# Kernel optimization log

Measured on AMD Instinct MI355X. Metric: run time of the kernel, lower is better.

The kernel has to match this reference:

```python
import jax, jax.numpy as jnp
import numpy as np

B, S, D, K, F = 4, 2048, 1024, 4, 4096
C_COEF = 8.0  # RG-LRU gating exponent from Griffin paper
EPS = 1e-6


def setup_inputs() -> dict:
    key = jax.random.key(0)
    ks = jax.random.split(key, 12)
    def n(k, shape, scale=1.0):
        return jax.random.normal(k, shape, dtype=jnp.float32) * scale
    sd = 1.0 / np.sqrt(D)
    return {
        "x": n(ks[0], (B, S, D)),
        "velocity": n(ks[1], (B, S, D), 0.1),
        "pre_norm_w": jnp.ones((D,), jnp.float32),
        "conv_kernel": n(ks[2], (D, K), 0.3),   # depthwise causal conv weights
        "conv_bias": jnp.zeros((D,), jnp.float32),
        "W_gate": n(ks[3], (D, D), sd),
        "W_a": n(ks[4], (D, D), sd),
        "lam": n(ks[5], (D,)),
        "W_out": n(ks[6], (2 * D, D), 1.0 / np.sqrt(2 * D)),
        "b_out": jnp.zeros((D,), jnp.float32),
        "log_beta": n(ks[7], (D,), 0.5),
        "ffn_norm_w": jnp.ones((D,), jnp.float32),
        "W_ff1": n(ks[8], (D, F), sd),
        "b_ff1": jnp.zeros((F,), jnp.float32),
        "W_ff2": n(ks[9], (F, D), 1.0 / np.sqrt(F)),
        "b_ff2": jnp.zeros((D,), jnp.float32),
    }


def _rmsnorm(x, w):
    # matches: rsqrt(x.float().pow(2).mean(-1, keepdim=True) + 1e-6); cast back; * weight
    xf = x.astype(jnp.float32)
    rms = jax.lax.rsqrt(jnp.mean(xf * xf, axis=-1, keepdims=True) + EPS)
    return (xf * rms).astype(x.dtype) * w


def _causal_dwconv(x, kernel, bias):
    # y[b,t,d] = bias[d] + sum_k kernel[d,k] * x[b,t-k,d]  (causal depthwise)
    k_taps = kernel.shape[1]
    s = x.shape[1]
    pad = jnp.pad(x, ((0, 0), (k_taps - 1, 0), (0, 0)))
    out = bias
    for k in range(k_taps):  # tiny fixed loop over kernel taps
        out = out + pad[:, k_taps - 1 - k : k_taps - 1 - k + s, :] * kernel[:, k]
    return out


def _griffin_scan(x, W_gate, W_a, lam):
    # RG-LRU: h_t = a_t * h_{t-1} + sqrt(1 - a_t^2) * (i_t * x_t)
    gate = jax.nn.sigmoid(jnp.einsum("bsd,de->bse", x, W_gate))
    log_a = -C_COEF * jax.nn.softplus(lam) * jax.nn.sigmoid(
        jnp.einsum("bsd,de->bse", x, W_a)
    )  # [B,S,D], log_a <= 0
    a = jnp.exp(log_a)
    u = jnp.sqrt(jnp.maximum(1.0 - a * a, 0.0)) * (gate * x)

    def step(h, au):
        a_t, u_t = au
        h = a_t * h + u_t
        return h, h

    a_t = jnp.moveaxis(a, 1, 0)  # [S,B,D]
    u_t = jnp.moveaxis(u, 1, 0)
    h0 = jnp.zeros_like(a_t[0])
    _, hs = jax.lax.scan(step, h0, (a_t, u_t))
    return jnp.moveaxis(hs, 0, 1)  # [B,S,D]


def reference(x, velocity, pre_norm_w, conv_kernel, conv_bias, W_gate, W_a, lam,
              W_out, b_out, log_beta, ffn_norm_w, W_ff1, b_ff1, W_ff2, b_ff2):
    x_norm = _rmsnorm(x, pre_norm_w)
    conv_out = _causal_dwconv(x_norm, conv_kernel, conv_bias)
    griffin_out = _griffin_scan(x_norm, W_gate, W_a, lam)
    mixer_out = jnp.concatenate([conv_out, griffin_out], axis=-1) @ W_out + b_out
    beta = jax.nn.sigmoid(log_beta)
    velocity = beta * velocity + mixer_out
    x = x + velocity
    normed = _rmsnorm(x, ffn_norm_w)
    ffn = jax.nn.gelu(normed @ W_ff1 + b_ff1) @ W_ff2 + b_ff2
    return (x + ffn, velocity)
```

## Files before the change

kernel.cpp:

```cpp
#include <hip/hip_runtime.h>

static constexpr int Bb = 4;
static constexpr int Ss = 2048;
static constexpr int Dd = 1024;
static constexpr int Ff = 4096;
static constexpr int Mm = Bb * Ss;
static constexpr size_t ND = (size_t)Mm * Dd;
static constexpr int CH = 32;
static constexpr int CL = Ss / CH;

typedef __attribute__((ext_vector_type(8))) short short8;
typedef __attribute__((ext_vector_type(4))) float floatx4;

__device__ __forceinline__ unsigned f2bf(float f) {
  unsigned u = __builtin_bit_cast(unsigned, f);
  return (u + 0x7FFFu + ((u >> 16) & 1u)) >> 16;
}
__device__ __forceinline__ float bf2f(unsigned bits) {
  return __builtin_bit_cast(float, bits << 16);
}
__device__ __forceinline__ void gload_lds16(const void* g, void* lds) {
  __builtin_amdgcn_global_load_lds((const __attribute__((address_space(1))) void*)g,
                                   (__attribute__((address_space(3))) void*)lds,
                                   16, 0, 0);
}
__device__ __forceinline__ float fsig(float x) {
  return __builtin_amdgcn_rcpf(1.0f + __expf(-x));
}
__device__ __forceinline__ float fgelu(float v) {
  float z = 1.5957691216057308f * fmaf(0.044715f * v, v * v, v);
  return v * __builtin_amdgcn_rcpf(1.0f + __expf(-z));
}

__global__ __launch_bounds__(256) void wconv_k(const float* __restrict__ W,
                                               unsigned short* __restrict__ WT,
                                               int K, int N) {
  __shared__ float tile[32][33];
  int tx = threadIdx.x & 31, ty = threadIdx.x >> 5;
  int bx = blockIdx.x * 32, by = blockIdx.y * 32;
#pragma unroll
  for (int i = 0; i < 32; i += 8)
    tile[ty + i][tx] = W[(size_t)(by + ty + i) * N + bx + tx];
  __syncthreads();
#pragma unroll
  for (int i = 0; i < 32; i += 8)
    WT[(size_t)(bx + ty + i) * K + by + tx] = (unsigned short)f2bf(tile[tx][ty + i]);
}

__global__ __launch_bounds__(256) void rmsnorm_bf_k(const float* __restrict__ x,
                                                    const float* __restrict__ w,
                                                    unsigned short* __restrict__ out) {
  int row = blockIdx.x;
  const float4* xr = (const float4*)(x + (size_t)row * Dd);
  int t = threadIdx.x;
  float4 v = xr[t];
  float ss = v.x * v.x + v.y * v.y + v.z * v.z + v.w * v.w;
#pragma unroll
  for (int off = 32; off > 0; off >>= 1) ss += __shfl_down(ss, off, 64);
  __shared__ float sb[4];
  if ((t & 63) == 0) sb[t >> 6] = ss;
  __syncthreads();
  float tot = sb[0] + sb[1] + sb[2] + sb[3];
  float sc = rsqrtf(tot * (1.0f / (float)Dd) + 1e-6f);
  float4 wv = ((const float4*)w)[t];
  unsigned lo = f2bf(v.x * sc * wv.x) | (f2bf(v.y * sc * wv.y) << 16);
  unsigned hi = f2bf(v.z * sc * wv.z) | (f2bf(v.w * sc * wv.w) << 16);
  *(uint2*)(out + (size_t)row * Dd + t * 4) = make_uint2(lo, hi);
}

__global__ __launch_bounds__(256) void conv_k(const unsigned short* __restrict__ xn,
                                              const float* __restrict__ kern,
                                              const float* __restrict__ bias,
                                              unsigned short* __restrict__ outC) {
  size_t q = (size_t)blockIdx.x * 256 + threadIdx.x;
  size_t i = q * 4;
  int d = (int)(i & (Dd - 1));
  int m = (int)(i >> 10);
  int t = m & (Ss - 1);
  float acc[4];
#pragma unroll
  for (int j = 0; j < 4; j++) acc[j] = bias[d + j];
#pragma unroll
  for (int k = 0; k < 4; k++) {
    if (t >= k) {
      uint2 xv = *(const uint2*)(xn + i - (size_t)k * Dd);
      float x0 = bf2f(xv.x & 0xFFFF), x1 = bf2f(xv.x >> 16);
      float x2 = bf2f(xv.y & 0xFFFF), x3 = bf2f(xv.y >> 16);
      acc[0] = fmaf(kern[(d + 0) * 4 + k], x0, acc[0]);
      acc[1] = fmaf(kern[(d + 1) * 4 + k], x1, acc[1]);
      acc[2] = fmaf(kern[(d + 2) * 4 + k], x2, acc[2]);
      acc[3] = fmaf(kern[(d + 3) * 4 + k], x3, acc[3]);
    }
  }
  unsigned lo = f2bf(acc[0]) | (f2bf(acc[1]) << 16);
  unsigned hi = f2bf(acc[2]) | (f2bf(acc[3]) << 16);
  *(uint2*)(outC + (size_t)m * (2 * Dd) + d) = make_uint2(lo, hi);
}

template <int MODE>
__global__ __launch_bounds__(512, 2) void bgemm3_k(const unsigned short* __restrict__ A,
                                                   const unsigned short* __restrict__ BT,
                                                   void* __restrict__ Cout,
                                                   int M, int N, int K,
                                                   const float* __restrict__ bias,
                                                   const float* __restrict__ extra,
                                                   const float* __restrict__ vel_in,
                                                   const float* __restrict__ x_in,
                                                   const float* __restrict__ log_beta,
                                                   float* __restrict__ vel_out) {
  __shared__ unsigned short LA[2][256 * 64];
  __shared__ unsigned short LB[2][256 * 64];
  const int tid = threadIdx.x;
  const int wid = tid >> 6, lane = tid & 63;
  const int wm = wid >> 2, wn = wid & 3;
  const int r = lane & 15, quad = lane >> 4, r7 = lane & 7;

  const int gx = gridDim.x;
  int id = blockIdx.y * gx + blockIdx.x;
  const int nwg = gx * gridDim.y;
  id = (id & 7) * (nwg >> 3) + (id >> 3);
  const int bm = (id / gx) * 256, bn = (id % gx) * 256;
  const int NIT = K >> 7;

  const int lrow = lane >> 3;
  const int sblk = (lane & 7) ^ lrow;
  const unsigned short* AsrcB = A  + (size_t)(bm + lrow) * K + sblk * 8;
  const unsigned short* BsrcB = BT + (size_t)(bn + lrow) * K + sblk * 8;

  const int aB = wm * 8192 + r * 64;
  const int bB = wn * 4096 + r * 64;
  const int kq0 = (quad ^ r7) * 8;
  const int kq1 = ((4 + quad) ^ r7) * 8;

  floatx4 acc[8][4];
#pragma unroll
  for (int i = 0; i < 8; i++)
#pragma unroll
    for (int j = 0; j < 4; j++) acc[i][j] = (floatx4){0.f, 0.f, 0.f, 0.f};

#define STG_A(bq, k0, h, s)                                                           \
  gload_lds16(AsrcB + (size_t)((h) * 128 + (s) * 64 + wid * 8) * K + (k0),            \
              (void*)&LA[bq][((h) * 128 + (s) * 64 + wid * 8) * 64])
#define STG_B(bq, k0, h, s)                                                           \
  gload_lds16(BsrcB + (size_t)((h) * 128 + (s) * 64 + wid * 8) * K + (k0),            \
              (void*)&LB[bq][((h) * 128 + (s) * 64 + wid * 8) * 64])
#define RDA(il, IH, buf)                                                              \
  aF[il][0] = *(const short8*)&LA[buf][aB + (IH) * 4096 + (il) * 1024 + kq0];         \
  aF[il][1] = *(const short8*)&LA[buf][aB + (IH) * 4096 + (il) * 1024 + kq1]
#define RDB(BF, jl, jg, buf)                                                          \
  BF[jl][0] = *(const short8*)&LB[buf][bB + (jg) * 1024 + kq0];                       \
  BF[jl][1] = *(const short8*)&LB[buf][bB + (jg) * 1024 + kq1]
#define MM2(il, jl, BF, IH, JH)                                                       \
  acc[(IH) * 4 + (il)][(JH) * 2 + (jl)] = __builtin_amdgcn_mfma_f32_16x16x32_bf16(    \
      BF[jl][0], aF[il][0], acc[(IH) * 4 + (il)][(JH) * 2 + (jl)], 0, 0, 0);          \
  acc[(IH) * 4 + (il)][(JH) * 2 + (jl)] = __builtin_amdgcn_mfma_f32_16x16x32_bf16(    \
      BF[jl][1], aF[il][1], acc[(IH) * 4 + (il)][(JH) * 2 + (jl)], 0, 0, 0)
#define MQUAD(BF, IH, JH)                                                             \
  MM2(0, 0, BF, IH, JH); MM2(0, 1, BF, IH, JH); MM2(1, 0, BF, IH, JH);                \
  MM2(1, 1, BF, IH, JH); MM2(2, 0, BF, IH, JH); MM2(2, 1, BF, IH, JH);                \
  MM2(3, 0, BF, IH, JH); MM2(3, 1, BF, IH, JH)
#define BAR() __builtin_amdgcn_s_barrier()
#define LGK0()                                                                        \
  asm volatile("s_waitcnt lgkmcnt(0)" ::: "memory");                                  \
  __builtin_amdgcn_sched_barrier(0)
#define PRIO(x) __builtin_amdgcn_s_setprio(x)

  STG_A(0, 0, 0, 0); STG_A(0, 0, 0, 1); STG_A(0, 0, 1, 0); STG_A(0, 0, 1, 1);
  STG_B(0, 0, 0, 0); STG_B(0, 0, 0, 1); STG_B(0, 0, 1, 0); STG_B(0, 0, 1, 1);
  STG_B(1, 64, 0, 0); STG_B(1, 64, 0, 1); STG_B(1, 64, 1, 0); STG_B(1, 64, 1, 1);
  asm volatile("s_waitcnt vmcnt(4)" ::: "memory");
  BAR();
  __builtin_amdgcn_sched_barrier(0);

  for (int it = 0; it < NIT; ++it) {
    const int T = 2 * it;
    const int pf = (it + 1 < NIT);
    const int kA1 = (T + 1) << 6;
    const int k2 = (T + 2) << 6, k3 = (T + 3) << 6;
    short8 aF[4][2], b0[2][2], b1[2][2];

    STG_A(1, kA1, 0, 0); STG_A(1, kA1, 0, 1);
    RDA(0, 0, 0); RDA(1, 0, 0); RDA(2, 0, 0); RDA(3, 0, 0);
    RDB(b0, 0, 0, 0); RDB(b0, 1, 1, 0);
    BAR(); LGK0();
    PRIO(1); MQUAD(b0, 0, 0); PRIO(0);
    BAR();

    STG_A(1, kA1, 1, 0); STG_A(1, kA1, 1, 1);
    RDB(b1, 0, 2, 0); RDB(b1, 1, 3, 0);
    BAR(); LGK0();
    PRIO(1); MQUAD(b1, 0, 1); PRIO(0);
    BAR();

    if (pf) { STG_B(0, k2, 0, 0); STG_B(0, k2, 0, 1); }
    RDA(0, 1, 0); RDA(1, 1, 0); RDA(2, 1, 0); RDA(3, 1, 0);
    BAR(); LGK0();
    PRIO(1); MQUAD(b0, 1, 0); PRIO(0);
    BAR();

    if (pf) { STG_B(0, k2, 1, 0); STG_B(0, k2, 1, 1); }
    BAR();
    PRIO(1); MQUAD(b1, 1, 1); PRIO(0);
    if (pf) asm volatile("s_waitcnt vmcnt(4)" ::: "memory");
    else    asm volatile("s_waitcnt vmcnt(0)" ::: "memory");
    BAR();
    __builtin_amdgcn_sched_barrier(0);

    if (pf) { STG_A(0, k2, 0, 0); STG_A(0, k2, 0, 1); }
    RDA(0, 0, 1); RDA(1, 0, 1); RDA(2, 0, 1); RDA(3, 0, 1);
    RDB(b0, 0, 0, 1); RDB(b0, 1, 1, 1);
    BAR(); LGK0();
    PRIO(1); MQUAD(b0, 0, 0); PRIO(0);
    BAR();

    if (pf) { STG_A(0, k2, 1, 0); STG_A(0, k2, 1, 1); }
    RDB(b1, 0, 2, 1); RDB(b1, 1, 3, 1);
    BAR(); LGK0();
    PRIO(1); MQUAD(b1, 0, 1); PRIO(0);
    BAR();

    if (pf) { STG_B(1, k3, 0, 0); STG_B(1, k3, 0, 1); }
    RDA(0, 1, 1); RDA(1, 1, 1); RDA(2, 1, 1); RDA(3, 1, 1);
    BAR(); LGK0();
    PRIO(1); MQUAD(b0, 1, 0); PRIO(0);
    BAR();

    if (pf) { STG_B(1, k3, 1, 0); STG_B(1, k3, 1, 1); }
    BAR();
    PRIO(1); MQUAD(b1, 1, 1); PRIO(0);
    if (pf) {
      asm volatile("s_waitcnt vmcnt(4)" ::: "memory");
      BAR();
      __builtin_amdgcn_sched_barrier(0);
    }
  }
#undef STG_A
#undef STG_B
#undef RDA
#undef RDB
#undef MM2
#undef MQUAD

#pragma unroll
  for (int i = 0; i < 8; i++) {
    int rowg = bm + wm * 128 + i * 16 + r;
#pragma unroll
    for (int j = 0; j < 4; j++) {
      int colg = bn + wn * 64 + j * 16 + quad * 4;
      size_t idx = (size_t)rowg * N + colg;
      float v0 = acc[i][j][0], v1 = acc[i][j][1], v2 = acc[i][j][2], v3 = acc[i][j][3];
      if (MODE & 1) {
        float4 bv = *(const float4*)(bias + colg);
        v0 += bv.x; v1 += bv.y; v2 += bv.z; v3 += bv.w;
      }
      if (MODE & 2) {
        v0 = fgelu(v0); v1 = fgelu(v1); v2 = fgelu(v2); v3 = fgelu(v3);
      }
      if (MODE & 4) {
        float4 ev = *(const float4*)(extra + idx);
        v0 += ev.x; v1 += ev.y; v2 += ev.z; v3 += ev.w;
      }
      if (MODE & 16) {
        float4 lb = *(const float4*)(log_beta + colg);
        float4 vi = *(const float4*)(vel_in + idx);
        float4 xi = *(const float4*)(x_in + idx);
        float4 vn;
        vn.x = fmaf(fsig(lb.x), vi.x, v0);
        vn.y = fmaf(fsig(lb.y), vi.y, v1);
        vn.z = fmaf(fsig(lb.z), vi.z, v2);
        vn.w = fmaf(fsig(lb.w), vi.w, v3);
        *(float4*)(vel_out + idx) = vn;
        v0 = xi.x + vn.x; v1 = xi.y + vn.y; v2 = xi.z + vn.z; v3 = xi.w + vn.w;
      }
      if (MODE & 8) {
        uint2 pk;
        pk.x = f2bf(v0) | (f2bf(v1) << 16);
        pk.y = f2bf(v2) | (f2bf(v3) << 16);
        *(uint2*)((unsigned short*)Cout + idx) = pk;
      } else {
        float4 o; o.x = v0; o.y = v1; o.z = v2; o.w = v3;
        *(float4*)((float*)Cout + idx) = o;
      }
    }
  }
}

template <int MODE>
__global__ __launch_bounds__(512, 2) void bgemm4_k(const unsigned short* __restrict__ A,
                                                   const unsigned short* __restrict__ BT,
                                                   void* __restrict__ Cout,
                                                   int M, int N, int K,
                                                   const float* __restrict__ bias,
                                                   const float* __restrict__ extra,
                                                   const float* __restrict__ vel_in,
                                                   const float* __restrict__ x_in,
                                                   const float* __restrict__ log_beta,
                                                   float* __restrict__ vel_out) {
  __shared__ unsigned short LA[2][256 * 64];
  __shared__ unsigned short LB[2][128 * 64];
  const int tid = threadIdx.x;
  const int wid = tid >> 6, lane = tid & 63;
  const int wm = wid >> 1, wn = wid & 1;
  const int r = lane & 15, quad = lane >> 4, r7 = lane & 7;

  const int gx = gridDim.x;
  int id = blockIdx.y * gx + blockIdx.x;
  const int nwg = gx * gridDim.y;
  id = (id & 7) * (nwg >> 3) + (id >> 3);
  const int bm = (id / gx) * 256, bn = (id % gx) * 128;
  const int NIT = K >> 7;

  const int lrow = lane >> 3;
  const int sblk = (lane & 7) ^ lrow;
  const unsigned short* AsrcB = A  + (size_t)(bm + lrow) * K + sblk * 8;
  const unsigned short* BsrcB = BT + (size_t)(bn + lrow) * K + sblk * 8;

  const int aB = wm * 4096 + r * 64;
  const int bB = wn * 4096 + r * 64;
  const int kq0 = (quad ^ r7) * 8;
  const int kq1 = ((4 + quad) ^ r7) * 8;

  floatx4 acc[4][4];
#pragma unroll
  for (int i = 0; i < 4; i++)
#pragma unroll
    for (int j = 0; j < 4; j++) acc[i][j] = (floatx4){0.f, 0.f, 0.f, 0.f};

#define STG_A4(bq, k0, h, s)                                                          \
  gload_lds16(AsrcB + (size_t)((h) * 128 + (s) * 64 + wid * 8) * K + (k0),            \
              (void*)&LA[bq][((h) * 128 + (s) * 64 + wid * 8) * 64])
#define STG_B4(bq, k0, s)                                                             \
  gload_lds16(BsrcB + (size_t)((s) * 64 + wid * 8) * K + (k0),                        \
              (void*)&LB[bq][((s) * 64 + wid * 8) * 64])
#define RDA4(IH, buf)                                                                 \
  aF[0][0] = *(const short8*)&LA[buf][aB + (IH) * 2048 + kq0];                        \
  aF[0][1] = *(const short8*)&LA[buf][aB + (IH) * 2048 + kq1];                        \
  aF[1][0] = *(const short8*)&LA[buf][aB + (IH) * 2048 + 1024 + kq0];                 \
  aF[1][1] = *(const short8*)&LA[buf][aB + (IH) * 2048 + 1024 + kq1]
#define RDB4(BF, JH, buf)                                                             \
  BF[0][0] = *(const short8*)&LB[buf][bB + (JH) * 2048 + kq0];                        \
  BF[0][1] = *(const short8*)&LB[buf][bB + (JH) * 2048 + kq1];                        \
  BF[1][0] = *(const short8*)&LB[buf][bB + (JH) * 2048 + 1024 + kq0];                 \
  BF[1][1] = *(const short8*)&LB[buf][bB + (JH) * 2048 + 1024 + kq1]
#define MM24(il, jl, BF, IH, JH)                                                      \
  acc[(IH) * 2 + (il)][(JH) * 2 + (jl)] = __builtin_amdgcn_mfma_f32_16x16x32_bf16(    \
      BF[jl][0], aF[il][0], acc[(IH) * 2 + (il)][(JH) * 2 + (jl)], 0, 0, 0);          \
  acc[(IH) * 2 + (il)][(JH) * 2 + (jl)] = __builtin_amdgcn_mfma_f32_16x16x32_bf16(    \
      BF[jl][1], aF[il][1], acc[(IH) * 2 + (il)][(JH) * 2 + (jl)], 0, 0, 0)
#define MQ4(BF, IH, JH)                                                               \
  MM24(0, 0, BF, IH, JH); MM24(0, 1, BF, IH, JH);                                     \
  MM24(1, 0, BF, IH, JH); MM24(1, 1, BF, IH, JH)

  STG_A4(0, 0, 0, 0); STG_A4(0, 0, 0, 1); STG_A4(0, 0, 1, 0); STG_A4(0, 0, 1, 1);
  STG_B4(0, 0, 0); STG_B4(0, 0, 1);
  STG_B4(1, 64, 0); STG_B4(1, 64, 1);
  asm volatile("s_waitcnt vmcnt(2)" ::: "memory");
  BAR();
  __builtin_amdgcn_sched_barrier(0);

  for (int it = 0; it < NIT; ++it) {
    const int T = 2 * it;
    const int pf = (it + 1 < NIT);
    const int kA1 = (T + 1) << 6;
    const int k2 = (T + 2) << 6, k3 = (T + 3) << 6;
    short8 aF[2][2], b0[2][2], b1[2][2];

    STG_A4(1, kA1, 0, 0); STG_A4(1, kA1, 0, 1);
    RDA4(0, 0); RDB4(b0, 0, 0);
    BAR(); LGK0();
    PRIO(1); MQ4(b0, 0, 0); PRIO(0);
    BAR();

    STG_A4(1, kA1, 1, 0); STG_A4(1, kA1, 1, 1);
    RDB4(b1, 1, 0);
    BAR(); LGK0();
    PRIO(1); MQ4(b1, 0, 1); PRIO(0);
    BAR();

    if (pf) STG_B4(0, k2, 0);
    RDA4(1, 0);
    BAR(); LGK0();
    PRIO(1); MQ4(b0, 1, 0); PRIO(0);
    BAR();

    if (pf) STG_B4(0, k2, 1);
    BAR();
    PRIO(1); MQ4(b1, 1, 1); PRIO(0);
    if (pf) asm volatile("s_waitcnt vmcnt(2)" ::: "memory");
    else    asm volatile("s_waitcnt vmcnt(0)" ::: "memory");
    BAR();
    __builtin_amdgcn_sched_barrier(0);

    if (pf) { STG_A4(0, k2, 0, 0); STG_A4(0, k2, 0, 1); }
    RDA4(0, 1); RDB4(b0, 0, 1);
    BAR(); LGK0();
    PRIO(1); MQ4(b0, 0, 0); PRIO(0);
    BAR();

    if (pf) { STG_A4(0, k2, 1, 0); STG_A4(0, k2, 1, 1); }
    RDB4(b1, 1, 1);
    BAR(); LGK0();
    PRIO(1); MQ4(b1, 0, 1); PRIO(0);
    BAR();

    if (pf) STG_B4(1, k3, 0);
    RDA4(1, 1);
    BAR(); LGK0();
    PRIO(1); MQ4(b0, 1, 0); PRIO(0);
    BAR();

    if (pf) STG_B4(1, k3, 1);
    BAR();
    PRIO(1); MQ4(b1, 1, 1); PRIO(0);
    if (pf) {
      asm volatile("s_waitcnt vmcnt(2)" ::: "memory");
      BAR();
      __builtin_amdgcn_sched_barrier(0);
    }
  }
#undef STG_A4
#undef STG_B4
#undef RDA4
#undef RDB4
#undef MM24
#undef MQ4
#undef BAR
#undef LGK0
#undef PRIO

#pragma unroll
  for (int i = 0; i < 4; i++) {
    int rowg = bm + wm * 64 + i * 16 + r;
#pragma unroll
    for (int j = 0; j < 4; j++) {
      int colg = bn + wn * 64 + j * 16 + quad * 4;
      size_t idx = (size_t)rowg * N + colg;
      float v0 = acc[i][j][0], v1 = acc[i][j][1], v2 = acc[i][j][2], v3 = acc[i][j][3];
      if (MODE & 1) {
        float4 bv = *(const float4*)(bias + colg);
        v0 += bv.x; v1 += bv.y; v2 += bv.z; v3 += bv.w;
      }
      if (MODE & 2) {
        v0 = fgelu(v0); v1 = fgelu(v1); v2 = fgelu(v2); v3 = fgelu(v3);
      }
      if (MODE & 4) {
        float4 ev = *(const float4*)(extra + idx);
        v0 += ev.x; v1 += ev.y; v2 += ev.z; v3 += ev.w;
      }
      if (MODE & 16) {
        float4 lb = *(const float4*)(log_beta + colg);
        float4 vi = *(const float4*)(vel_in + idx);
        float4 xi = *(const float4*)(x_in + idx);
        float4 vn;
        vn.x = fmaf(fsig(lb.x), vi.x, v0);
        vn.y = fmaf(fsig(lb.y), vi.y, v1);
        vn.z = fmaf(fsig(lb.z), vi.z, v2);
        vn.w = fmaf(fsig(lb.w), vi.w, v3);
        *(float4*)(vel_out + idx) = vn;
        v0 = xi.x + vn.x; v1 = xi.y + vn.y; v2 = xi.z + vn.z; v3 = xi.w + vn.w;
      }
      if (MODE & 8) {
        uint2 pk;
        pk.x = f2bf(v0) | (f2bf(v1) << 16);
        pk.y = f2bf(v2) | (f2bf(v3) << 16);
        *(uint2*)((unsigned short*)Cout + idx) = pk;
      } else {
        float4 o; o.x = v0; o.y = v1; o.z = v2; o.w = v3;
        *(float4*)((float*)Cout + idx) = o;
      }
    }
  }
}

__global__ __launch_bounds__(256) void scan_p1(const unsigned short* __restrict__ gapre,
                                               const unsigned short* __restrict__ xn,
                                               const float* __restrict__ lam,
                                               unsigned short* __restrict__ ub,
                                               float* __restrict__ carryA,
                                               float* __restrict__ carryH) {
  int g = blockIdx.x * 256 + threadIdx.x;
  int e = g & (Dd - 1);
  int bc = g >> 10;
  int b = bc & 3;
  int c = bc >> 2;
  float l = lam[e];
  float sp = fmaxf(l, 0.0f) + log1pf(__expf(-fabsf(l)));
  float m8sp = -8.0f * sp;
  size_t m0 = (size_t)b * Ss + (size_t)c * CL;
  float A = 1.0f, h = 0.0f;
#pragma unroll 4
  for (int t = 0; t < CL; t++) {
    size_t m = m0 + t;
    float gp = bf2f(gapre[m * 2048 + e]);
    float ap = bf2f(gapre[m * 2048 + 1024 + e]);
    float xv = bf2f(xn[m * Dd + e]);
    float a = __expf(m8sp * fsig(ap));
    float u = sqrtf(fmaxf(1.0f - a * a, 0.0f)) * fsig(gp) * xv;
    ub[m * Dd + e] = (unsigned short)f2bf(u);
    A *= a;
    h = fmaf(a, h, u);
  }
  carryA[c * 4096 + b * 1024 + e] = A;
  carryH[c * 4096 + b * 1024 + e] = h;
}

__global__ __launch_bounds__(256) void scan_p2(const float* __restrict__ carryA,
                                               const float* __restrict__ carryH,
                                               float* __restrict__ init) {
  int ch = blockIdx.x * 256 + threadIdx.x;
  float H = 0.0f;
#pragma unroll
  for (int c = 0; c < CH; c++) {
    init[c * 4096 + ch] = H;
    H = fmaf(carryA[c * 4096 + ch], H, carryH[c * 4096 + ch]);
  }
}

__global__ __launch_bounds__(256) void scan_p3(const unsigned short* __restrict__ gapre,
                                               const unsigned short* __restrict__ ub,
                                               const float* __restrict__ lam,
                                               const float* __restrict__ init,
                                               unsigned short* __restrict__ outC) {
  int g = blockIdx.x * 256 + threadIdx.x;
  int e = g & (Dd - 1);
  int bc = g >> 10;
  int b = bc & 3;
  int c = bc >> 2;
  float l = lam[e];
  float sp = fmaxf(l, 0.0f) + log1pf(__expf(-fabsf(l)));
  float m8sp = -8.0f * sp;
  size_t m0 = (size_t)b * Ss + (size_t)c * CL;
  float h = init[c * 4096 + b * 1024 + e];
#pragma unroll 4
  for (int t = 0; t < CL; t++) {
    size_t m = m0 + t;
    float ap = bf2f(gapre[m * 2048 + 1024 + e]);
    float a = __expf(m8sp * fsig(ap));
    float u = bf2f(ub[m * Dd + e]);
    h = fmaf(a, h, u);
    outC[m * (2 * Dd) + Dd + e] = (unsigned short)f2bf(h);
  }
}

extern "C" void kernel_launch(void* const* d_in, const int* in_sizes, int n_in,
                              void* d_out, int out_size, void* d_ws, size_t ws_size,
                              hipStream_t stream) {
  const float* x        = (const float*)d_in[0];
  const float* velocity = (const float*)d_in[1];
  const float* pre_w    = (const float*)d_in[2];
  const float* conv_w   = (const float*)d_in[3];
  const float* conv_b   = (const float*)d_in[4];
  const float* W_gate   = (const float*)d_in[5];
  const float* W_a      = (const float*)d_in[6];
  const float* lam      = (const float*)d_in[7];
  const float* W_out    = (const float*)d_in[8];
  const float* b_out    = (const float*)d_in[9];
  const float* log_beta = (const float*)d_in[10];
  const float* ffn_w    = (const float*)d_in[11];
  const float* W_ff1    = (const float*)d_in[12];
  const float* b_ff1    = (const float*)d_in[13];
  const float* W_ff2    = (const float*)d_in[14];
  const float* b_ff2    = (const float*)d_in[15];

  float* out0 = (float*)d_out;
  float* out1 = out0 + ND;

  const size_t MB = 1024 * 1024;
  char* ws = (char*)d_ws;
  unsigned short* WgaT  = (unsigned short*)ws;
  unsigned short* WoT   = WgaT + (size_t)2 * 1024 * 1024;
  unsigned short* Wf1T  = WoT + (size_t)2 * 1024 * 1024;
  unsigned short* Wf2T  = Wf1T + (size_t)4 * 1024 * 1024;
  float*          mixer = (float*)(ws + 24 * MB);
  float*          carA  = (float*)(ws + 24 * MB);
  float*          carH  = (float*)(ws + 24 * MB + 512 * 1024);
  float*          initb = (float*)(ws + 25 * MB);
  unsigned short* conc  = (unsigned short*)(ws + 56 * MB);
  unsigned short* gapre = (unsigned short*)(ws + 88 * MB);
  unsigned short* xnbf  = (unsigned short*)(ws + 120 * MB);
  unsigned short* ubf   = (unsigned short*)(ws + 136 * MB);
  unsigned short* midbf = (unsigned short*)(ws + 88 * MB);
  unsigned short* nrmbf = (unsigned short*)(ws + 56 * MB);

  const int EB = 256;
  const int egrid4 = (int)(ND / 4 / EB);

  wconv_k<<<dim3(32, 32),  256, 0, stream>>>(W_gate, WgaT, 1024, 1024);
  wconv_k<<<dim3(32, 32),  256, 0, stream>>>(W_a,    WgaT + (size_t)1024 * 1024, 1024, 1024);
  wconv_k<<<dim3(32, 64),  256, 0, stream>>>(W_out,  WoT, 2048, 1024);
  wconv_k<<<dim3(128, 32), 256, 0, stream>>>(W_ff1,  Wf1T, 1024, 4096);
  wconv_k<<<dim3(32, 128), 256, 0, stream>>>(W_ff2,  Wf2T, 4096, 1024);
  rmsnorm_bf_k<<<Mm, 256, 0, stream>>>(x, pre_w, xnbf);
  conv_k<<<egrid4, EB, 0, stream>>>(xnbf, conv_w, conv_b, conc);
  bgemm3_k<8><<<dim3(8, 32), 512, 0, stream>>>(xnbf, WgaT, gapre, Mm, 2048, 1024,
      nullptr, nullptr, nullptr, nullptr, nullptr, nullptr);
  scan_p1<<<512, 256, 0, stream>>>(gapre, xnbf, lam, ubf, carA, carH);
  scan_p2<<<16, 256, 0, stream>>>(carA, carH, initb);
  scan_p3<<<512, 256, 0, stream>>>(gapre, ubf, lam, initb, conc);
  bgemm4_k<1 | 16><<<dim3(8, 32), 512, 0, stream>>>(conc, WoT, mixer, Mm, 1024, 2048,
      b_out, nullptr, velocity, x, log_beta, out1);
  rmsnorm_bf_k<<<Mm, 256, 0, stream>>>(mixer, ffn_w, nrmbf);
  bgemm3_k<1 | 2 | 8><<<dim3(16, 32), 512, 0, stream>>>(nrmbf, Wf1T, midbf, Mm, 4096, 1024,
      b_ff1, nullptr, nullptr, nullptr, nullptr, nullptr);
  bgemm4_k<1 | 4><<<dim3(8, 32), 512, 0, stream>>>(midbf, Wf2T, out0, Mm, 1024, 4096,
      b_ff2, mixer, nullptr, nullptr, nullptr, nullptr);
}
```

Baseline: 587.3 us.

## Triple-buffer A tile in bgemm4 kernel with rotating LDS slots

Makes the A operand LDS staging in the 256x128 GEMM kernel a three-slot ring instead of two, so A tiles are prefetched two K-steps ahead. Each half-iteration now issues two MQ4 blocks per barrier phase instead of one, halving the number of barrier/lgkm wait points per K-step. This is meant to hide global-to-LDS latency and cut synchronisation overhead. In exchange LDS use grows by 32 KB per block (to 128 KB), which may limit occupancy at launch_bounds(512,2), and more B fragments are held in registers at once.

```diff
diff --git a/kernel.cpp b/kernel.cpp
--- a/kernel.cpp
+++ b/kernel.cpp
@@ -296,7 +296,7 @@
                                                    const float* __restrict__ x_in,
                                                    const float* __restrict__ log_beta,
                                                    float* __restrict__ vel_out) {
-  __shared__ unsigned short LA[2][256 * 64];
+  __shared__ unsigned short LA[3][256 * 64];
   __shared__ unsigned short LB[2][128 * 64];
   const int tid = threadIdx.x;
   const int wid = tid >> 6, lane = tid & 63;
@@ -315,6 +315,10 @@
   const unsigned short* AsrcB = A  + (size_t)(bm + lrow) * K + sblk * 8;
   const unsigned short* BsrcB = BT + (size_t)(bn + lrow) * K + sblk * 8;
 
+  unsigned short* ALDS = &LA[0][0];
+  unsigned short* B0 = &LB[0][0];
+  unsigned short* B1 = &LB[1][0];
+
   const int aB = wm * 4096 + r * 64;
   const int bB = wn * 4096 + r * 64;
   const int kq0 = (quad ^ r7) * 8;
@@ -326,104 +330,91 @@
 #pragma unroll
     for (int j = 0; j < 4; j++) acc[i][j] = (floatx4){0.f, 0.f, 0.f, 0.f};
 
-#define STG_A4(bq, k0, h, s)                                                          \
+#define STG_A6(dst, k0, h, s)                                                         \
   gload_lds16(AsrcB + (size_t)((h) * 128 + (s) * 64 + wid * 8) * K + (k0),            \
-              (void*)&LA[bq][((h) * 128 + (s) * 64 + wid * 8) * 64])
-#define STG_B4(bq, k0, s)                                                             \
+              (void*)((dst) + ((h) * 128 + (s) * 64 + wid * 8) * 64))
+#define STG_B6(dst, k0, s)                                                            \
   gload_lds16(BsrcB + (size_t)((s) * 64 + wid * 8) * K + (k0),                        \
-              (void*)&LB[bq][((s) * 64 + wid * 8) * 64])
-#define RDA4(IH, buf)                                                                 \
-  aF[0][0] = *(const short8*)&LA[buf][aB + (IH) * 2048 + kq0];                        \
-  aF[0][1] = *(const short8*)&LA[buf][aB + (IH) * 2048 + kq1];                        \
-  aF[1][0] = *(const short8*)&LA[buf][aB + (IH) * 2048 + 1024 + kq0];                 \
-  aF[1][1] = *(const short8*)&LA[buf][aB + (IH) * 2048 + 1024 + kq1]
-#define RDB4(BF, JH, buf)                                                             \
-  BF[0][0] = *(const short8*)&LB[buf][bB + (JH) * 2048 + kq0];                        \
-  BF[0][1] = *(const short8*)&LB[buf][bB + (JH) * 2048 + kq1];                        \
-  BF[1][0] = *(const short8*)&LB[buf][bB + (JH) * 2048 + 1024 + kq0];                 \
-  BF[1][1] = *(const short8*)&LB[buf][bB + (JH) * 2048 + 1024 + kq1]
-#define MM24(il, jl, BF, IH, JH)                                                      \
+              (void*)((dst) + ((s) * 64 + wid * 8) * 64))
+#define RDA6(src, IH)                                                                 \
+  aF[0][0] = *(const short8*)((src) + aB + (IH) * 2048 + kq0);                        \
+  aF[0][1] = *(const short8*)((src) + aB + (IH) * 2048 + kq1);                        \
+  aF[1][0] = *(const short8*)((src) + aB + (IH) * 2048 + 1024 + kq0);                 \
+  aF[1][1] = *(const short8*)((src) + aB + (IH) * 2048 + 1024 + kq1)
+#define RDB6(BF, src, JH)                                                             \
+  BF[0][0] = *(const short8*)((src) + bB + (JH) * 2048 + kq0);                        \
+  BF[0][1] = *(const short8*)((src) + bB + (JH) * 2048 + kq1);                        \
+  BF[1][0] = *(const short8*)((src) + bB + (JH) * 2048 + 1024 + kq0);                 \
+  BF[1][1] = *(const short8*)((src) + bB + (JH) * 2048 + 1024 + kq1)
+#define MM26(il, jl, BF, IH, JH)                                                      \
   acc[(IH) * 2 + (il)][(JH) * 2 + (jl)] = __builtin_amdgcn_mfma_f32_16x16x32_bf16(    \
       BF[jl][0], aF[il][0], acc[(IH) * 2 + (il)][(JH) * 2 + (jl)], 0, 0, 0);          \
   acc[(IH) * 2 + (il)][(JH) * 2 + (jl)] = __builtin_amdgcn_mfma_f32_16x16x32_bf16(    \
       BF[jl][1], aF[il][1], acc[(IH) * 2 + (il)][(JH) * 2 + (jl)], 0, 0, 0)
-#define MQ4(BF, IH, JH)                                                               \
-  MM24(0, 0, BF, IH, JH); MM24(0, 1, BF, IH, JH);                                     \
-  MM24(1, 0, BF, IH, JH); MM24(1, 1, BF, IH, JH)
-
-  STG_A4(0, 0, 0, 0); STG_A4(0, 0, 0, 1); STG_A4(0, 0, 1, 0); STG_A4(0, 0, 1, 1);
-  STG_B4(0, 0, 0); STG_B4(0, 0, 1);
-  STG_B4(1, 64, 0); STG_B4(1, 64, 1);
-  asm volatile("s_waitcnt vmcnt(2)" ::: "memory");
+#define MQ6(BF, IH, JH)                                                               \
+  MM26(0, 0, BF, IH, JH); MM26(0, 1, BF, IH, JH);                                     \
+  MM26(1, 0, BF, IH, JH); MM26(1, 1, BF, IH, JH)
+
+  STG_A6(ALDS, 0, 0, 0); STG_A6(ALDS, 0, 0, 1); STG_A6(ALDS, 0, 1, 0); STG_A6(ALDS, 0, 1, 1);
+  STG_B6(B0, 0, 0); STG_B6(B0, 0, 1);
+  STG_A6(ALDS + 16384, 64, 0, 0); STG_A6(ALDS + 16384, 64, 0, 1);
+  STG_A6(ALDS + 16384, 64, 1, 0); STG_A6(ALDS + 16384, 64, 1, 1);
+  STG_B6(B1, 64, 0); STG_B6(B1, 64, 1);
+  asm volatile("s_waitcnt vmcnt(6)" ::: "memory");
   BAR();
   __builtin_amdgcn_sched_barrier(0);
 
+  int p = 0;
   for (int it = 0; it < NIT; ++it) {
     const int T = 2 * it;
     const int pf = (it + 1 < NIT);
-    const int kA1 = (T + 1) << 6;
     const int k2 = (T + 2) << 6, k3 = (T + 3) << 6;
-    short8 aF[2][2], b0[2][2], b1[2][2];
-
-    STG_A4(1, kA1, 0, 0); STG_A4(1, kA1, 0, 1);
-    RDA4(0, 0); RDB4(b0, 0, 0);
-    BAR(); LGK0();
-    PRIO(1); MQ4(b0, 0, 0); PRIO(0);
-    BAR();
-
-    STG_A4(1, kA1, 1, 0); STG_A4(1, kA1, 1, 1);
-    RDB4(b1, 1, 0);
-    BAR(); LGK0();
-    PRIO(1); MQ4(b1, 0, 1); PRIO(0);
-    BAR();
-
-    if (pf) STG_B4(0, k2, 0);
-    RDA4(1, 0);
-    BAR(); LGK0();
-    PRIO(1); MQ4(b0, 1, 0); PRIO(0);
-    BAR();
-
-    if (pf) STG_B4(0, k2, 1);
-    BAR();
-    PRIO(1); MQ4(b1, 1, 1); PRIO(0);
-    if (pf) asm volatile("s_waitcnt vmcnt(2)" ::: "memory");
+    const int pn = (p == 2) ? 0 : p + 1;
+    const int p2 = (pn == 2) ? 0 : pn + 1;
+    unsigned short* Acur = ALDS + p * 16384;
+    unsigned short* Anxt = ALDS + pn * 16384;
+    unsigned short* Asg2 = ALDS + p2 * 16384;
+    short8 aF[2][2], bR0[2][2], bR1[2][2];
+
+    if (pf) { STG_A6(Asg2, k2, 0, 0); STG_A6(Asg2, k2, 0, 1); }
+    RDA6(Acur, 0); RDB6(bR0, B0, 0); RDB6(bR1, B0, 1);
+    BAR(); LGK0();
+    PRIO(1); MQ6(bR0, 0, 0); MQ6(bR1, 0, 1); PRIO(0);
+    BAR();
+
+    if (pf) { STG_A6(Asg2, k2, 1, 0); STG_A6(Asg2, k2, 1, 1); STG_B6(B0, k2, 0); }
+    RDA6(Acur, 1);
+    BAR(); LGK0();
+    PRIO(1); MQ6(bR0, 1, 0); MQ6(bR1, 1, 1); PRIO(0);
+    if (pf) asm volatile("s_waitcnt vmcnt(5)" ::: "memory");
     else    asm volatile("s_waitcnt vmcnt(0)" ::: "memory");
     BAR();
     __builtin_amdgcn_sched_barrier(0);
 
-    if (pf) { STG_A4(0, k2, 0, 0); STG_A4(0, k2, 0, 1); }
-    RDA4(0, 1); RDB4(b0, 0, 1);
-    BAR(); LGK0();
-    PRIO(1); MQ4(b0, 0, 0); PRIO(0);
-    BAR();
-
-    if (pf) { STG_A4(0, k2, 1, 0); STG_A4(0, k2, 1, 1); }
-    RDB4(b1, 1, 1);
-    BAR(); LGK0();
-    PRIO(1); MQ4(b1, 0, 1); PRIO(0);
-    BAR();
-
-    if (pf) STG_B4(1, k3, 0);
-    RDA4(1, 1);
-    BAR(); LGK0();
-    PRIO(1); MQ4(b0, 1, 0); PRIO(0);
-    BAR();
-
-    if (pf) STG_B4(1, k3, 1);
-    BAR();
-    PRIO(1); MQ4(b1, 1, 1); PRIO(0);
+    if (pf) { STG_B6(B0, k2, 1); STG_A6(Acur, k3, 0, 0); STG_A6(Acur, k3, 0, 1); }
+    RDA6(Anxt, 0); RDB6(bR0, B1, 0); RDB6(bR1, B1, 1);
+    BAR(); LGK0();
+    PRIO(1); MQ6(bR0, 0, 0); MQ6(bR1, 0, 1); PRIO(0);
+    BAR();
+
+    if (pf) { STG_A6(Acur, k3, 1, 0); STG_A6(Acur, k3, 1, 1);
+              STG_B6(B1, k3, 0); STG_B6(B1, k3, 1); }
+    RDA6(Anxt, 1);
+    BAR(); LGK0();
+    PRIO(1); MQ6(bR0, 1, 0); MQ6(bR1, 1, 1); PRIO(0);
     if (pf) {
-      asm volatile("s_waitcnt vmcnt(2)" ::: "memory");
+      asm volatile("s_waitcnt vmcnt(6)" ::: "memory");
       BAR();
       __builtin_amdgcn_sched_barrier(0);
     }
-  }
-#undef STG_A4
-#undef STG_B4
-#undef RDA4
-#undef RDB4
-#undef MM24
-#undef MQ4
+    p = p2;
+  }
+#undef STG_A6
+#undef STG_B6
+#undef RDA6
+#undef RDB6
+#undef MM26
+#undef MQ6
 #undef BAR
 #undef LGK0
 #undef PRIO
```

After: 616.8 us. 5.0% more time.
